# Kernel tuning notes

Hardware: AMD Instinct MI355X
Metric: run time of the kernel (lower is better)

Reference implementation:

```python
import jax, jax.numpy as jnp
import numpy as np

TOP_K = 2

def setup_inputs() -> dict:
    key = jax.random.key(0)
    k1, k2, k3 = jax.random.split(key, 3)
    B, S, H, E = 4, 4096, 4096, 64
    return {
        "hidden_states": jax.random.normal(k1, (B, S, H), dtype=jnp.float32),
        "weight": jax.random.normal(k2, (E, H), dtype=jnp.float32),
        "bias": jax.random.normal(k3, (E,), dtype=jnp.float32),
    }

def reference(hidden_states, weight, bias):
    B, S, H = hidden_states.shape
    E = weight.shape[0]
    x = hidden_states.reshape(-1, H)                      # [N, H]
    router_logits = jnp.einsum('nh,eh->ne', x, weight) + bias  # [N, E]
    routing_weights, selected_experts = jax.lax.top_k(router_logits, TOP_K)
    routing_weights = jax.nn.softmax(routing_weights.astype(jnp.float32), axis=-1).astype(hidden_states.dtype)
    N = x.shape[0]
    rows = jnp.arange(N)[:, None]
    final = jnp.zeros((N, E), dtype=router_logits.dtype).at[rows, selected_experts].set(routing_weights)
    return final.reshape(B, S, E), selected_experts
```

## Files before the change

### kernel.cpp

```cpp
#include <hip/hip_runtime.h>
#include <math.h>


constexpr int E_EXPERTS = 64;
constexpr int H_DIM = 4096;
constexpr int BLOCK = 512;
constexpr int ROWS_B = 64;
constexpr int NSTEP = 64;
constexpr int KHALF = 2048;
constexpr int SROW = 40;
constexpr int PSTR = E_EXPERTS * SROW;
constexpr int QSTR = 3 * PSTR;
constexpr int BSTR = 2 * QSTR;
constexpr int W_ELEMS = E_EXPERTS * H_DIM;

typedef __attribute__((ext_vector_type(8))) short short8;
typedef __attribute__((ext_vector_type(4))) float f32x4;

__device__ __forceinline__ float4 ld4(const float* p) {
  return *reinterpret_cast<const float4*>(p);
}
__device__ __forceinline__ short8 lds8(const unsigned short* p) {
  return *reinterpret_cast<const short8*>(p);
}

__device__ __forceinline__ unsigned short bf_rne(float x) {
  unsigned u = __builtin_bit_cast(unsigned, x);
  return (unsigned short)((u + 0x7fffu + ((u >> 16) & 1u)) >> 16);
}
__device__ __forceinline__ float bf2f(unsigned short b) {
  return __builtin_bit_cast(float, ((unsigned)b) << 16);
}
__device__ __forceinline__ void split3(float x, unsigned short& h,
                                       unsigned short& m, unsigned short& l) {
  unsigned short hb = (unsigned short)(__builtin_bit_cast(unsigned, x) >> 16);
  float r1 = x - bf2f(hb);
  unsigned short mb = (unsigned short)(__builtin_bit_cast(unsigned, r1) >> 16);
  float r2 = r1 - bf2f(mb);
  h = hb;
  m = mb;
  l = bf_rne(r2);
}
__device__ __forceinline__ void split3_8(float4 a, float4 b, short8& h,
                                         short8& m, short8& l) {
  unsigned short hh, mm, ll;
  split3(a.x, hh, mm, ll); h[0] = (short)hh; m[0] = (short)mm; l[0] = (short)ll;
  split3(a.y, hh, mm, ll); h[1] = (short)hh; m[1] = (short)mm; l[1] = (short)ll;
  split3(a.z, hh, mm, ll); h[2] = (short)hh; m[2] = (short)mm; l[2] = (short)ll;
  split3(a.w, hh, mm, ll); h[3] = (short)hh; m[3] = (short)mm; l[3] = (short)ll;
  split3(b.x, hh, mm, ll); h[4] = (short)hh; m[4] = (short)mm; l[4] = (short)ll;
  split3(b.y, hh, mm, ll); h[5] = (short)hh; m[5] = (short)mm; l[5] = (short)ll;
  split3(b.z, hh, mm, ll); h[6] = (short)hh; m[6] = (short)mm; l[6] = (short)ll;
  split3(b.w, hh, mm, ll); h[7] = (short)hh; m[7] = (short)mm; l[7] = (short)ll;
}

__global__ __launch_bounds__(256) void split_w_kernel(
    const float* __restrict__ w, unsigned short* __restrict__ wh,
    unsigned short* __restrict__ wm, unsigned short* __restrict__ wl) {
  const int i = (blockIdx.x * 256 + threadIdx.x) * 4;
  float4 v = ld4(w + i);
  ushort4 h4, m4, l4;
  split3(v.x, h4.x, m4.x, l4.x);
  split3(v.y, h4.y, m4.y, l4.y);
  split3(v.z, h4.z, m4.z, l4.z);
  split3(v.w, h4.w, m4.w, l4.w);
  *reinterpret_cast<ushort4*>(wh + i) = h4;
  *reinterpret_cast<ushort4*>(wm + i) = m4;
  *reinterpret_cast<ushort4*>(wl + i) = l4;
}

__global__ __launch_bounds__(BLOCK, 2) void topk_router_mfma(
    const float* __restrict__ x, const unsigned short* __restrict__ wh,
    const unsigned short* __restrict__ wm,
    const unsigned short* __restrict__ wl, const float* __restrict__ bias,
    float* __restrict__ out_final, float* __restrict__ out_idx) {
  __shared__ short smem[2 * BSTR];

  const int tid = threadIdx.x;
  const int lane = tid & 63;
  const int wid = tid >> 6;
  const int rg = wid & 3;
  const int kq = wid >> 2;
  const int rowBase = blockIdx.x * ROWS_B;
  const int lr = lane & 15;
  const int kg = lane >> 4;

  const int sw = tid & 255;
  const int se = sw >> 2;
  const int sk8 = tid & 3;
  const int skq = tid >> 8;
  const size_t gbase = (size_t)se * H_DIM + skq * KHALF + sk8 * 8;
  const int lbase = skq * QSTR + se * SROW + sk8 * 8;

  const float* __restrict__ xp =
      x + (size_t)(rowBase + rg * 16 + lr) * H_DIM + kq * KHALF + kg * 8;

  short8 s0, s1, s2;
  float4 xA0, xA1, xB0, xB1;

  f32x4 acc0 = {0.f, 0.f, 0.f, 0.f}, acc1 = acc0, acc2 = acc0, acc3 = acc0;

#define SLOAD(s)                        \
  do {                                  \
    const size_t go = gbase + (s) * 32; \
    s0 = lds8(wh + go);                 \
    s1 = lds8(wm + go);                 \
    s2 = lds8(wl + go);                 \
  } while (0)

#define SWRITE(buf)                                                         \
  do {                                                                      \
    *reinterpret_cast<short8*>(&smem[(buf)*BSTR + lbase + 0 * PSTR]) = s0;  \
    *reinterpret_cast<short8*>(&smem[(buf)*BSTR + lbase + 1 * PSTR]) = s1;  \
    *reinterpret_cast<short8*>(&smem[(buf)*BSTR + lbase + 2 * PSTR]) = s2;  \
  } while (0)

#define XLOAD(d0, d1, s)                  \
  do {                                    \
    d0 = ld4(xp + (size_t)(s) * 32);      \
    d1 = ld4(xp + (size_t)(s) * 32 + 4);  \
  } while (0)

  SLOAD(0);
  SWRITE(0);
  SLOAD(1);
  XLOAD(xA0, xA1, 0);
  XLOAD(xB0, xB1, 1);
  __syncthreads();

  const int fbase = kq * QSTR + lr * SROW + kg * 8;

#define FRAGS(buf, g, p)                      \
  (*reinterpret_cast<const short8*>(          \
      &smem[(buf)*BSTR + fbase + (g)*16 * SROW + (p)*PSTR]))

#define MM(d, a, b) d = __builtin_amdgcn_mfma_f32_16x16x32_bf16(a, b, d, 0, 0, 0)
#define PROD6(d, Ah, Am, Al, Bh, Bm, Bl)                      \
  MM(d, Ah, Bh); MM(d, Ah, Bm); MM(d, Am, Bh); MM(d, Am, Bm); \
  MM(d, Ah, Bl); MM(d, Al, Bh)

#define PHASE(s, buf, XF0, XF1)                                     \
  do {                                                              \
    if ((s) + 1 < NSTEP) SWRITE(1 - (buf));  \
    if ((s) + 2 < NSTEP) SLOAD((s) + 2);     \
    short8 b0h = FRAGS(buf, 0, 0), b0m = FRAGS(buf, 0, 1),          \
           b0l = FRAGS(buf, 0, 2);                                  \
    short8 b1h = FRAGS(buf, 1, 0), b1m = FRAGS(buf, 1, 1),          \
           b1l = FRAGS(buf, 1, 2);                                  \
    short8 b2h = FRAGS(buf, 2, 0), b2m = FRAGS(buf, 2, 1),          \
           b2l = FRAGS(buf, 2, 2);                                  \
    short8 b3h = FRAGS(buf, 3, 0), b3m = FRAGS(buf, 3, 1),          \
           b3l = FRAGS(buf, 3, 2);                                  \
    short8 ah, am, al;                                              \
    split3_8(XF0, XF1, ah, am, al);                                 \
    if ((s) + 2 < NSTEP) XLOAD(XF0, XF1, (s) + 2);                  \
    PROD6(acc0, ah, am, al, b0h, b0m, b0l);                         \
    PROD6(acc1, ah, am, al, b1h, b1m, b1l);                         \
    PROD6(acc2, ah, am, al, b2h, b2m, b2l);                         \
    PROD6(acc3, ah, am, al, b3h, b3m, b3l);                         \
    __syncthreads();                                                \
  } while (0)

  for (int s = 0; s < NSTEP; s += 2) {
    PHASE(s, 0, xA0, xA1);
    PHASE(s + 1, 1, xB0, xB1);
  }

  float* part = reinterpret_cast<float*>(smem);
  const int pr = kg * 4;
#define PSTORE(A, g)                                                       \
  part[((size_t)kq * 64 + rg * 16 + pr + 0) * 68 + (g)*16 + lr] = A[0];    \
  part[((size_t)kq * 64 + rg * 16 + pr + 1) * 68 + (g)*16 + lr] = A[1];    \
  part[((size_t)kq * 64 + rg * 16 + pr + 2) * 68 + (g)*16 + lr] = A[2];    \
  part[((size_t)kq * 64 + rg * 16 + pr + 3) * 68 + (g)*16 + lr] = A[3];
  PSTORE(acc0, 0)
  PSTORE(acc1, 1)
  PSTORE(acc2, 2)
  PSTORE(acc3, 3)
  __syncthreads();

  const int r = tid >> 3;
  const int eb = (tid & 7) * 8;
  const int n = rowBase + r;

  float v8[8];
#pragma unroll
  for (int j = 0; j < 8; ++j) {
    int e = eb + j;
    v8[j] = (part[(size_t)r * 68 + e] + part[(size_t)(64 + r) * 68 + e]) +
            bias[e];
  }

  float av = -INFINITY, bv = -INFINITY;
  int ai = E_EXPERTS, bi = E_EXPERTS;
#pragma unroll
  for (int j = 0; j < 8; ++j) {
    int e = eb + j;
    float v = v8[j];
    bool beats_a = (v > av) || (v == av && e < ai);
    bool beats_b = (v > bv) || (v == bv && e < bi);
    if (beats_a) {
      bv = av; bi = ai; av = v; ai = e;
    } else if (beats_b) {
      bv = v; bi = e;
    }
  }
#pragma unroll
  for (int d = 1; d < 8; d <<= 1) {
    float av2 = __shfl_xor(av, d);
    float bv2 = __shfl_xor(bv, d);
    int ai2 = __shfl_xor(ai, d);
    int bi2 = __shfl_xor(bi, d);
    bool afirst = (av > av2) || (av == av2 && ai < ai2);
    float na, nb;
    int nai, nbi;
    if (afirst) {
      na = av; nai = ai;
      bool t = (bv > av2) || (bv == av2 && bi < ai2);
      nb = t ? bv : av2;
      nbi = t ? bi : ai2;
    } else {
      na = av2; nai = ai2;
      bool t = (av > bv2) || (av == bv2 && ai < bi2);
      nb = t ? av : bv2;
      nbi = t ? ai : bi2;
    }
    av = na; ai = nai; bv = nb; bi = nbi;
  }

  float e1 = expf(bv - av);
  float denom = 1.0f + e1;
  float p0 = 1.0f / denom;
  float p1 = e1 / denom;

#pragma unroll
  for (int i = 0; i < 2; ++i) {
    float4 o4;
    float* po = &o4.x;
#pragma unroll
    for (int j = 0; j < 4; ++j) {
      int e = eb + i * 4 + j;
      po[j] = (e == ai) ? p0 : (e == bi) ? p1 : 0.0f;
    }
    *reinterpret_cast<float4*>(&out_final[(size_t)n * E_EXPERTS + eb + i * 4]) =
        o4;
  }
  if ((tid & 7) == 0) {
    out_idx[(size_t)n * 2 + 0] = (float)ai;
    out_idx[(size_t)n * 2 + 1] = (float)bi;
  }
}

extern "C" void kernel_launch(void* const* d_in, const int* in_sizes, int n_in,
                              void* d_out, int out_size, void* d_ws,
                              size_t ws_size, hipStream_t stream) {
  const float* x = (const float*)d_in[0];
  const float* w = (const float*)d_in[1];
  const float* bias = (const float*)d_in[2];
  const int N = in_sizes[0] / H_DIM;
  float* out_final = (float*)d_out;
  float* out_idx = out_final + (size_t)N * E_EXPERTS;

  unsigned short* wh = (unsigned short*)d_ws;
  unsigned short* wm = wh + W_ELEMS;
  unsigned short* wl = wm + W_ELEMS;

  split_w_kernel<<<W_ELEMS / (256 * 4), 256, 0, stream>>>(w, wh, wm, wl);
  topk_router_mfma<<<N / ROWS_B, BLOCK, 0, stream>>>(x, wh, wm, wl, bias,
                                                     out_final, out_idx);
}
```

Measured before the change: 102.6 us.

## Drop LDS weight staging; read split weights directly from global per wave

Blocks shrink to 16 rows and 256 threads, with each of 4 waves covering a 1024-wide K slice. Each wave loads the bf16 hi/mid/lo weight fragments straight from global memory (L2-resident) instead of staging them through double-buffered LDS with barriers. This removes the LDS writes and the per-step __syncthreads, and raises the block count from 256 to 1024. The cost is much less weight reuse per block: each block rereads the full split weight from cache, so L2 traffic grows by about 4x. The partial sums are reduced across 4 K-slices and the top-k shuffle reduction now spans 16 lanes.

```diff
diff --git a/kernel.cpp b/kernel.cpp
--- a/kernel.cpp
+++ b/kernel.cpp
@@ -4,14 +4,10 @@
 
 constexpr int E_EXPERTS = 64;
 constexpr int H_DIM = 4096;
-constexpr int BLOCK = 512;
-constexpr int ROWS_B = 64;
-constexpr int NSTEP = 64;
-constexpr int KHALF = 2048;
-constexpr int SROW = 40;
-constexpr int PSTR = E_EXPERTS * SROW;
-constexpr int QSTR = 3 * PSTR;
-constexpr int BSTR = 2 * QSTR;
+constexpr int BLOCK = 256;
+constexpr int ROWS_B = 16;
+constexpr int KSLICE = 1024;
+constexpr int NCH = 32;
 constexpr int W_ELEMS = E_EXPERTS * H_DIM;
 
 typedef __attribute__((ext_vector_type(8))) short short8;
@@ -69,134 +65,154 @@
   *reinterpret_cast<ushort4*>(wl + i) = l4;
 }
 
-__global__ __launch_bounds__(BLOCK, 2) void topk_router_mfma(
+__global__ __launch_bounds__(BLOCK, 4) void topk_router_mfma(
     const float* __restrict__ x, const unsigned short* __restrict__ wh,
     const unsigned short* __restrict__ wm,
     const unsigned short* __restrict__ wl, const float* __restrict__ bias,
     float* __restrict__ out_final, float* __restrict__ out_idx) {
-  __shared__ short smem[2 * BSTR];
+  __shared__ float part[4 * ROWS_B * 68];
 
   const int tid = threadIdx.x;
   const int lane = tid & 63;
-  const int wid = tid >> 6;
-  const int rg = wid & 3;
-  const int kq = wid >> 2;
+  const int kq = tid >> 6;
   const int rowBase = blockIdx.x * ROWS_B;
   const int lr = lane & 15;
   const int kg = lane >> 4;
 
-  const int sw = tid & 255;
-  const int se = sw >> 2;
-  const int sk8 = tid & 3;
-  const int skq = tid >> 8;
-  const size_t gbase = (size_t)se * H_DIM + skq * KHALF + sk8 * 8;
-  const int lbase = skq * QSTR + se * SROW + sk8 * 8;
-
-  const float* __restrict__ xp =
-      x + (size_t)(rowBase + rg * 16 + lr) * H_DIM + kq * KHALF + kg * 8;
-
-  short8 s0, s1, s2;
+  const size_t wo = (size_t)lr * H_DIM + kq * KSLICE + kg * 8;
+  const unsigned short* __restrict__ whp = wh + wo;
+  const unsigned short* __restrict__ wmp = wm + wo;
+  const unsigned short* __restrict__ wlp = wl + wo;
+
+  const float* __restrict__ xr =
+      x + (size_t)(rowBase + lr) * H_DIM + kq * KSLICE + kg * 8;
+
   float4 xA0, xA1, xB0, xB1;
+#define XLOADA(t)                         \
+  do {                                    \
+    xA0 = ld4(xr + (size_t)(t) * 32);     \
+    xA1 = ld4(xr + (size_t)(t) * 32 + 4); \
+  } while (0)
+#define XLOADB(t)                         \
+  do {                                    \
+    xB0 = ld4(xr + (size_t)(t) * 32);     \
+    xB1 = ld4(xr + (size_t)(t) * 32 + 4); \
+  } while (0)
 
   f32x4 acc0 = {0.f, 0.f, 0.f, 0.f}, acc1 = acc0, acc2 = acc0, acc3 = acc0;
-
-#define SLOAD(s)                        \
-  do {                                  \
-    const size_t go = gbase + (s) * 32; \
-    s0 = lds8(wh + go);                 \
-    s1 = lds8(wm + go);                 \
-    s2 = lds8(wl + go);                 \
-  } while (0)
-
-#define SWRITE(buf)                                                         \
-  do {                                                                      \
-    *reinterpret_cast<short8*>(&smem[(buf)*BSTR + lbase + 0 * PSTR]) = s0;  \
-    *reinterpret_cast<short8*>(&smem[(buf)*BSTR + lbase + 1 * PSTR]) = s1;  \
-    *reinterpret_cast<short8*>(&smem[(buf)*BSTR + lbase + 2 * PSTR]) = s2;  \
-  } while (0)
-
-#define XLOAD(d0, d1, s)                  \
-  do {                                    \
-    d0 = ld4(xp + (size_t)(s) * 32);      \
-    d1 = ld4(xp + (size_t)(s) * 32 + 4);  \
-  } while (0)
-
-  SLOAD(0);
-  SWRITE(0);
-  SLOAD(1);
-  XLOAD(xA0, xA1, 0);
-  XLOAD(xB0, xB1, 1);
-  __syncthreads();
-
-  const int fbase = kq * QSTR + lr * SROW + kg * 8;
-
-#define FRAGS(buf, g, p)                      \
-  (*reinterpret_cast<const short8*>(          \
-      &smem[(buf)*BSTR + fbase + (g)*16 * SROW + (p)*PSTR]))
 
 #define MM(d, a, b) d = __builtin_amdgcn_mfma_f32_16x16x32_bf16(a, b, d, 0, 0, 0)
 #define PROD6(d, Ah, Am, Al, Bh, Bm, Bl)                      \
   MM(d, Ah, Bh); MM(d, Ah, Bm); MM(d, Am, Bh); MM(d, Am, Bm); \
   MM(d, Ah, Bl); MM(d, Al, Bh)
 
-#define PHASE(s, buf, XF0, XF1)                                     \
-  do {                                                              \
-    if ((s) + 1 < NSTEP) SWRITE(1 - (buf));  \
-    if ((s) + 2 < NSTEP) SLOAD((s) + 2);     \
-    short8 b0h = FRAGS(buf, 0, 0), b0m = FRAGS(buf, 0, 1),          \
-           b0l = FRAGS(buf, 0, 2);                                  \
-    short8 b1h = FRAGS(buf, 1, 0), b1m = FRAGS(buf, 1, 1),          \
-           b1l = FRAGS(buf, 1, 2);                                  \
-    short8 b2h = FRAGS(buf, 2, 0), b2m = FRAGS(buf, 2, 1),          \
-           b2l = FRAGS(buf, 2, 2);                                  \
-    short8 b3h = FRAGS(buf, 3, 0), b3m = FRAGS(buf, 3, 1),          \
-           b3l = FRAGS(buf, 3, 2);                                  \
-    short8 ah, am, al;                                              \
-    split3_8(XF0, XF1, ah, am, al);                                 \
-    if ((s) + 2 < NSTEP) XLOAD(XF0, XF1, (s) + 2);                  \
-    PROD6(acc0, ah, am, al, b0h, b0m, b0l);                         \
-    PROD6(acc1, ah, am, al, b1h, b1m, b1l);                         \
-    PROD6(acc2, ah, am, al, b2h, b2m, b2l);                         \
-    PROD6(acc3, ah, am, al, b3h, b3m, b3l);                         \
-    __syncthreads();                                                \
+#define CHUNK(c, X0, X1)                                           \
+  do {                                                             \
+    const size_t o_ = (size_t)(c) * 32;                            \
+    short8 b0h = lds8(whp + o_);                                   \
+    short8 b1h = lds8(whp + o_ + (size_t)16 * H_DIM);              \
+    short8 b2h = lds8(whp + o_ + (size_t)32 * H_DIM);              \
+    short8 b3h = lds8(whp + o_ + (size_t)48 * H_DIM);              \
+    short8 b0m = lds8(wmp + o_);                                   \
+    short8 b1m = lds8(wmp + o_ + (size_t)16 * H_DIM);              \
+    short8 b2m = lds8(wmp + o_ + (size_t)32 * H_DIM);              \
+    short8 b3m = lds8(wmp + o_ + (size_t)48 * H_DIM);              \
+    short8 b0l = lds8(wlp + o_);                                   \
+    short8 b1l = lds8(wlp + o_ + (size_t)16 * H_DIM);              \
+    short8 b2l = lds8(wlp + o_ + (size_t)32 * H_DIM);              \
+    short8 b3l = lds8(wlp + o_ + (size_t)48 * H_DIM);              \
+    short8 ah, am, al;                                             \
+    split3_8(X0, X1, ah, am, al);                                  \
+    PROD6(acc0, ah, am, al, b0h, b0m, b0l);                        \
+    PROD6(acc1, ah, am, al, b1h, b1m, b1l);                        \
+    PROD6(acc2, ah, am, al, b2h, b2m, b2l);                        \
+    PROD6(acc3, ah, am, al, b3h, b3m, b3l);                        \
   } while (0)
 
-  for (int s = 0; s < NSTEP; s += 2) {
-    PHASE(s, 0, xA0, xA1);
-    PHASE(s + 1, 1, xB0, xB1);
-  }
-
-  float* part = reinterpret_cast<float*>(smem);
+  XLOADA(0);
+  XLOADB(1);
+
+  for (int c = 0; c < NCH; c += 2) {
+    {
+      const size_t o_ = (size_t)c * 32;
+      short8 b0h = lds8(whp + o_);
+      short8 b1h = lds8(whp + o_ + (size_t)16 * H_DIM);
+      short8 b2h = lds8(whp + o_ + (size_t)32 * H_DIM);
+      short8 b3h = lds8(whp + o_ + (size_t)48 * H_DIM);
+      short8 b0m = lds8(wmp + o_);
+      short8 b1m = lds8(wmp + o_ + (size_t)16 * H_DIM);
+      short8 b2m = lds8(wmp + o_ + (size_t)32 * H_DIM);
+      short8 b3m = lds8(wmp + o_ + (size_t)48 * H_DIM);
+      short8 b0l = lds8(wlp + o_);
+      short8 b1l = lds8(wlp + o_ + (size_t)16 * H_DIM);
+      short8 b2l = lds8(wlp + o_ + (size_t)32 * H_DIM);
+      short8 b3l = lds8(wlp + o_ + (size_t)48 * H_DIM);
+      short8 ah, am, al;
+      split3_8(xA0, xA1, ah, am, al);
+      if (c + 2 < NCH) XLOADA(c + 2);
+      PROD6(acc0, ah, am, al, b0h, b0m, b0l);
+      PROD6(acc1, ah, am, al, b1h, b1m, b1l);
+      PROD6(acc2, ah, am, al, b2h, b2m, b2l);
+      PROD6(acc3, ah, am, al, b3h, b3m, b3l);
+    }
+    {
+      const size_t o_ = (size_t)(c + 1) * 32;
+      short8 b0h = lds8(whp + o_);
+      short8 b1h = lds8(whp + o_ + (size_t)16 * H_DIM);
+      short8 b2h = lds8(whp + o_ + (size_t)32 * H_DIM);
+      short8 b3h = lds8(whp + o_ + (size_t)48 * H_DIM);
+      short8 b0m = lds8(wmp + o_);
+      short8 b1m = lds8(wmp + o_ + (size_t)16 * H_DIM);
+      short8 b2m = lds8(wmp + o_ + (size_t)32 * H_DIM);
+      short8 b3m = lds8(wmp + o_ + (size_t)48 * H_DIM);
+      short8 b0l = lds8(wlp + o_);
+      short8 b1l = lds8(wlp + o_ + (size_t)16 * H_DIM);
+      short8 b2l = lds8(wlp + o_ + (size_t)32 * H_DIM);
+      short8 b3l = lds8(wlp + o_ + (size_t)48 * H_DIM);
+      short8 ah, am, al;
+      split3_8(xB0, xB1, ah, am, al);
+      if (c + 3 < NCH) XLOADB(c + 3);
+      PROD6(acc0, ah, am, al, b0h, b0m, b0l);
+      PROD6(acc1, ah, am, al, b1h, b1m, b1l);
+      PROD6(acc2, ah, am, al, b2h, b2m, b2l);
+      PROD6(acc3, ah, am, al, b3h, b3m, b3l);
+    }
+  }
+
   const int pr = kg * 4;
-#define PSTORE(A, g)                                                       \
-  part[((size_t)kq * 64 + rg * 16 + pr + 0) * 68 + (g)*16 + lr] = A[0];    \
-  part[((size_t)kq * 64 + rg * 16 + pr + 1) * 68 + (g)*16 + lr] = A[1];    \
-  part[((size_t)kq * 64 + rg * 16 + pr + 2) * 68 + (g)*16 + lr] = A[2];    \
-  part[((size_t)kq * 64 + rg * 16 + pr + 3) * 68 + (g)*16 + lr] = A[3];
+#define PSTORE(A, g)                                          \
+  part[(size_t)(kq * 16 + pr + 0) * 68 + (g)*16 + lr] = A[0]; \
+  part[(size_t)(kq * 16 + pr + 1) * 68 + (g)*16 + lr] = A[1]; \
+  part[(size_t)(kq * 16 + pr + 2) * 68 + (g)*16 + lr] = A[2]; \
+  part[(size_t)(kq * 16 + pr + 3) * 68 + (g)*16 + lr] = A[3];
   PSTORE(acc0, 0)
   PSTORE(acc1, 1)
   PSTORE(acc2, 2)
   PSTORE(acc3, 3)
   __syncthreads();
 
-  const int r = tid >> 3;
-  const int eb = (tid & 7) * 8;
+  const int r = tid >> 4;
+  const int te = tid & 15;
+  const int eb = te * 4;
   const int n = rowBase + r;
 
-  float v8[8];
-#pragma unroll
-  for (int j = 0; j < 8; ++j) {
+  float v4[4];
+#pragma unroll
+  for (int j = 0; j < 4; ++j) {
     int e = eb + j;
-    v8[j] = (part[(size_t)r * 68 + e] + part[(size_t)(64 + r) * 68 + e]) +
+    v4[j] = ((part[(size_t)(0 * 16 + r) * 68 + e] +
+              part[(size_t)(1 * 16 + r) * 68 + e]) +
+             (part[(size_t)(2 * 16 + r) * 68 + e] +
+              part[(size_t)(3 * 16 + r) * 68 + e])) +
             bias[e];
   }
 
   float av = -INFINITY, bv = -INFINITY;
   int ai = E_EXPERTS, bi = E_EXPERTS;
 #pragma unroll
-  for (int j = 0; j < 8; ++j) {
+  for (int j = 0; j < 4; ++j) {
     int e = eb + j;
-    float v = v8[j];
+    float v = v4[j];
     bool beats_a = (v > av) || (v == av && e < ai);
     bool beats_b = (v > bv) || (v == bv && e < bi);
     if (beats_a) {
@@ -206,7 +222,7 @@
     }
   }
 #pragma unroll
-  for (int d = 1; d < 8; d <<= 1) {
+  for (int d = 1; d < 16; d <<= 1) {
     float av2 = __shfl_xor(av, d);
     float bv2 = __shfl_xor(bv, d);
     int ai2 = __shfl_xor(ai, d);
@@ -233,19 +249,17 @@
   float p0 = 1.0f / denom;
   float p1 = e1 / denom;
 
-#pragma unroll
-  for (int i = 0; i < 2; ++i) {
+  {
     float4 o4;
     float* po = &o4.x;
 #pragma unroll
     for (int j = 0; j < 4; ++j) {
-      int e = eb + i * 4 + j;
+      int e = eb + j;
       po[j] = (e == ai) ? p0 : (e == bi) ? p1 : 0.0f;
     }
-    *reinterpret_cast<float4*>(&out_final[(size_t)n * E_EXPERTS + eb + i * 4]) =
-        o4;
-  }
-  if ((tid & 7) == 0) {
+    *reinterpret_cast<float4*>(&out_final[(size_t)n * E_EXPERTS + eb]) = o4;
+  }
+  if (te == 0) {
     out_idx[(size_t)n * 2 + 0] = (float)ai;
     out_idx[(size_t)n * 2 + 1] = (float)bi;
   }
```

New measurement: 219.9 us. +114.4%, slower.

## Split K across all eight waves with per-wave async LDS staging of weight planes

Applied to the files above, without the earlier changes.

Each of the 8 waves now owns a 512-wide K slice and computes the full 64x64 tile with 16 accumulators, instead of 4 row groups by 2 K halves. Weight hi/mid planes are copied straight into per-wave LDS buffers with global_load_lds and explicit vmcnt waits. The low plane is read directly from global, and block-wide syncs inside the loop are dropped. Partial sums from all eight K slices are reduced in shared memory at the end. The goal is less sync overhead and more reuse of A and B fragments per wave, at the cost of higher register pressure and a bigger final reduction.

```diff
diff --git a/kernel.cpp b/kernel.cpp
--- a/kernel.cpp
+++ b/kernel.cpp
@@ -6,13 +6,11 @@
 constexpr int H_DIM = 4096;
 constexpr int BLOCK = 512;
 constexpr int ROWS_B = 64;
-constexpr int NSTEP = 64;
-constexpr int KHALF = 2048;
-constexpr int SROW = 40;
-constexpr int PSTR = E_EXPERTS * SROW;
-constexpr int QSTR = 3 * PSTR;
-constexpr int BSTR = 2 * QSTR;
+constexpr int KSLICE = 512;
+constexpr int NCH = 16;
 constexpr int W_ELEMS = E_EXPERTS * H_DIM;
+constexpr int TILE_SH = 8 * 512;
+constexpr int WAVE_SH = 2 * TILE_SH;
 
 typedef __attribute__((ext_vector_type(8))) short short8;
 typedef __attribute__((ext_vector_type(4))) float f32x4;
@@ -22,6 +20,12 @@
 }
 __device__ __forceinline__ short8 lds8(const unsigned short* p) {
   return *reinterpret_cast<const short8*>(p);
+}
+__device__ __forceinline__ void gload16(const unsigned short* g,
+                                        unsigned short* l) {
+  __builtin_amdgcn_global_load_lds(
+      (const __attribute__((address_space(1))) void*)g,
+      (__attribute__((address_space(3))) void*)l, 16, 0, 0);
 }
 
 __device__ __forceinline__ unsigned short bf_rne(float x) {
@@ -70,113 +74,143 @@
 }
 
 __global__ __launch_bounds__(BLOCK, 2) void topk_router_mfma(
-    const float* __restrict__ x, const unsigned short* __restrict__ wh,
-    const unsigned short* __restrict__ wm,
-    const unsigned short* __restrict__ wl, const float* __restrict__ bias,
-    float* __restrict__ out_final, float* __restrict__ out_idx) {
-  __shared__ short smem[2 * BSTR];
+    const float* __restrict__ x, const unsigned short* __restrict__ wplanes,
+    const float* __restrict__ bias, float* __restrict__ out_final,
+    float* __restrict__ out_idx) {
+  __shared__ f32x4 smem4[8704];
+  unsigned short* sbase = reinterpret_cast<unsigned short*>(smem4);
+  float* part = reinterpret_cast<float*>(smem4);
 
   const int tid = threadIdx.x;
   const int lane = tid & 63;
-  const int wid = tid >> 6;
-  const int rg = wid & 3;
-  const int kq = wid >> 2;
+  const int kq = tid >> 6;
   const int rowBase = blockIdx.x * ROWS_B;
   const int lr = lane & 15;
   const int kg = lane >> 4;
 
-  const int sw = tid & 255;
-  const int se = sw >> 2;
-  const int sk8 = tid & 3;
-  const int skq = tid >> 8;
-  const size_t gbase = (size_t)se * H_DIM + skq * KHALF + sk8 * 8;
-  const int lbase = skq * QSTR + se * SROW + sk8 * 8;
-
-  const float* __restrict__ xp =
-      x + (size_t)(rowBase + rg * 16 + lr) * H_DIM + kq * KHALF + kg * 8;
-
-  short8 s0, s1, s2;
-  float4 xA0, xA1, xB0, xB1;
-
-  f32x4 acc0 = {0.f, 0.f, 0.f, 0.f}, acc1 = acc0, acc2 = acc0, acc3 = acc0;
-
-#define SLOAD(s)                        \
-  do {                                  \
-    const size_t go = gbase + (s) * 32; \
-    s0 = lds8(wh + go);                 \
-    s1 = lds8(wm + go);                 \
-    s2 = lds8(wl + go);                 \
+  unsigned short* lb = sbase + kq * WAVE_SH;
+
+  const unsigned short* __restrict__ wb =
+      wplanes + (size_t)lr * H_DIM + kq * KSLICE + kg * 8;
+  const unsigned short* __restrict__ wlb = wb + (size_t)2 * W_ELEMS;
+
+#define STAGE(t, buf)                                                       \
+  do {                                                                      \
+    const size_t o_ = (size_t)(t) * 32;                                     \
+    unsigned short* d_ = lb + (buf)*TILE_SH;                                \
+    gload16(wb + o_, d_ + 0 * 512);                                         \
+    gload16(wb + o_ + (size_t)W_ELEMS, d_ + 1 * 512);                       \
+    gload16(wb + o_ + (size_t)16 * H_DIM, d_ + 2 * 512);                    \
+    gload16(wb + o_ + (size_t)16 * H_DIM + (size_t)W_ELEMS, d_ + 3 * 512);  \
+    gload16(wb + o_ + (size_t)32 * H_DIM, d_ + 4 * 512);                    \
+    gload16(wb + o_ + (size_t)32 * H_DIM + (size_t)W_ELEMS, d_ + 5 * 512);  \
+    gload16(wb + o_ + (size_t)48 * H_DIM, d_ + 6 * 512);                    \
+    gload16(wb + o_ + (size_t)48 * H_DIM + (size_t)W_ELEMS, d_ + 7 * 512);  \
   } while (0)
 
-#define SWRITE(buf)                                                         \
-  do {                                                                      \
-    *reinterpret_cast<short8*>(&smem[(buf)*BSTR + lbase + 0 * PSTR]) = s0;  \
-    *reinterpret_cast<short8*>(&smem[(buf)*BSTR + lbase + 1 * PSTR]) = s1;  \
-    *reinterpret_cast<short8*>(&smem[(buf)*BSTR + lbase + 2 * PSTR]) = s2;  \
+  const float* __restrict__ xr0 =
+      x + (size_t)(rowBase + lr) * H_DIM + kq * KSLICE + kg * 8;
+  const float* __restrict__ xr1 = xr0 + (size_t)16 * H_DIM;
+  const float* __restrict__ xr2 = xr0 + (size_t)32 * H_DIM;
+  const float* __restrict__ xr3 = xr0 + (size_t)48 * H_DIM;
+
+  float4 xA00, xA01, xA10, xA11, xA20, xA21, xA30, xA31;
+  float4 xB00, xB01, xB10, xB11, xB20, xB21, xB30, xB31;
+#define XLOADA(t)                                                         \
+  do {                                                                    \
+    xA00 = ld4(xr0 + (size_t)(t) * 32); xA01 = ld4(xr0 + (size_t)(t) * 32 + 4); \
+    xA10 = ld4(xr1 + (size_t)(t) * 32); xA11 = ld4(xr1 + (size_t)(t) * 32 + 4); \
+    xA20 = ld4(xr2 + (size_t)(t) * 32); xA21 = ld4(xr2 + (size_t)(t) * 32 + 4); \
+    xA30 = ld4(xr3 + (size_t)(t) * 32); xA31 = ld4(xr3 + (size_t)(t) * 32 + 4); \
   } while (0)
-
-#define XLOAD(d0, d1, s)                  \
-  do {                                    \
-    d0 = ld4(xp + (size_t)(s) * 32);      \
-    d1 = ld4(xp + (size_t)(s) * 32 + 4);  \
+#define XLOADB(t)                                                         \
+  do {                                                                    \
+    xB00 = ld4(xr0 + (size_t)(t) * 32); xB01 = ld4(xr0 + (size_t)(t) * 32 + 4); \
+    xB10 = ld4(xr1 + (size_t)(t) * 32); xB11 = ld4(xr1 + (size_t)(t) * 32 + 4); \
+    xB20 = ld4(xr2 + (size_t)(t) * 32); xB21 = ld4(xr2 + (size_t)(t) * 32 + 4); \
+    xB30 = ld4(xr3 + (size_t)(t) * 32); xB31 = ld4(xr3 + (size_t)(t) * 32 + 4); \
   } while (0)
 
-  SLOAD(0);
-  SWRITE(0);
-  SLOAD(1);
-  XLOAD(xA0, xA1, 0);
-  XLOAD(xB0, xB1, 1);
-  __syncthreads();
-
-  const int fbase = kq * QSTR + lr * SROW + kg * 8;
-
-#define FRAGS(buf, g, p)                      \
-  (*reinterpret_cast<const short8*>(          \
-      &smem[(buf)*BSTR + fbase + (g)*16 * SROW + (p)*PSTR]))
+  f32x4 c00 = {0.f, 0.f, 0.f, 0.f}, c01 = c00, c02 = c00, c03 = c00,
+        c10 = c00, c11 = c00, c12 = c00, c13 = c00, c20 = c00, c21 = c00,
+        c22 = c00, c23 = c00, c30 = c00, c31 = c00, c32 = c00, c33 = c00;
 
 #define MM(d, a, b) d = __builtin_amdgcn_mfma_f32_16x16x32_bf16(a, b, d, 0, 0, 0)
 #define PROD6(d, Ah, Am, Al, Bh, Bm, Bl)                      \
   MM(d, Ah, Bh); MM(d, Ah, Bm); MM(d, Am, Bh); MM(d, Am, Bm); \
   MM(d, Ah, Bl); MM(d, Al, Bh)
 
-#define PHASE(s, buf, XF0, XF1)                                     \
-  do {                                                              \
-    if ((s) + 1 < NSTEP) SWRITE(1 - (buf));  \
-    if ((s) + 2 < NSTEP) SLOAD((s) + 2);     \
-    short8 b0h = FRAGS(buf, 0, 0), b0m = FRAGS(buf, 0, 1),          \
-           b0l = FRAGS(buf, 0, 2);                                  \
-    short8 b1h = FRAGS(buf, 1, 0), b1m = FRAGS(buf, 1, 1),          \
-           b1l = FRAGS(buf, 1, 2);                                  \
-    short8 b2h = FRAGS(buf, 2, 0), b2m = FRAGS(buf, 2, 1),          \
-           b2l = FRAGS(buf, 2, 2);                                  \
-    short8 b3h = FRAGS(buf, 3, 0), b3m = FRAGS(buf, 3, 1),          \
-           b3l = FRAGS(buf, 3, 2);                                  \
-    short8 ah, am, al;                                              \
-    split3_8(XF0, XF1, ah, am, al);                                 \
-    if ((s) + 2 < NSTEP) XLOAD(XF0, XF1, (s) + 2);                  \
-    PROD6(acc0, ah, am, al, b0h, b0m, b0l);                         \
-    PROD6(acc1, ah, am, al, b1h, b1m, b1l);                         \
-    PROD6(acc2, ah, am, al, b2h, b2m, b2l);                         \
-    PROD6(acc3, ah, am, al, b3h, b3m, b3l);                         \
-    __syncthreads();                                                \
+  STAGE(0, 0);
+  XLOADA(0);
+  XLOADB(1);
+
+#define BODY(c, X00, X01, X10, X11, X20, X21, X30, X31, XLOADM)              \
+  do {                                                                       \
+    if ((c) + 1 < NCH) STAGE((c) + 1, ((c) + 1) & 1);                        \
+    const size_t wo_ = (size_t)(c) * 32;                                     \
+    short8 bl0 = lds8(wlb + wo_);                                            \
+    short8 bl1 = lds8(wlb + wo_ + (size_t)16 * H_DIM);                       \
+    short8 bl2 = lds8(wlb + wo_ + (size_t)32 * H_DIM);                       \
+    short8 bl3 = lds8(wlb + wo_ + (size_t)48 * H_DIM);                       \
+    __builtin_amdgcn_sched_barrier(0);                                       \
+    if ((c) == 0) {                                                          \
+      asm volatile("s_waitcnt vmcnt(28)" ::: "memory");                      \
+    } else if ((c) <= 14) {                                                  \
+      asm volatile("s_waitcnt vmcnt(20)" ::: "memory");                      \
+    } else {                                                                 \
+      asm volatile("s_waitcnt vmcnt(0)" ::: "memory");                       \
+    }                                                                        \
+    __builtin_amdgcn_sched_barrier(0);                                       \
+    const unsigned short* tb_ = lb + ((c)&1) * TILE_SH;                      \
+    short8 b0h = lds8(tb_ + 0 * 512 + lane * 8);                             \
+    short8 b0m = lds8(tb_ + 1 * 512 + lane * 8);                             \
+    short8 b1h = lds8(tb_ + 2 * 512 + lane * 8);                             \
+    short8 b1m = lds8(tb_ + 3 * 512 + lane * 8);                             \
+    short8 b2h = lds8(tb_ + 4 * 512 + lane * 8);                             \
+    short8 b2m = lds8(tb_ + 5 * 512 + lane * 8);                             \
+    short8 b3h = lds8(tb_ + 6 * 512 + lane * 8);                             \
+    short8 b3m = lds8(tb_ + 7 * 512 + lane * 8);                             \
+    short8 a0h, a0m, a0l, a1h, a1m, a1l, a2h, a2m, a2l, a3h, a3m, a3l;       \
+    split3_8(X00, X01, a0h, a0m, a0l);                                       \
+    split3_8(X10, X11, a1h, a1m, a1l);                                       \
+    split3_8(X20, X21, a2h, a2m, a2l);                                       \
+    split3_8(X30, X31, a3h, a3m, a3l);                                       \
+    if ((c) + 2 < NCH) XLOADM((c) + 2);          \
+    PROD6(c00, a0h, a0m, a0l, b0h, b0m, bl0);                                \
+    PROD6(c01, a0h, a0m, a0l, b1h, b1m, bl1);                                \
+    PROD6(c02, a0h, a0m, a0l, b2h, b2m, bl2);                                \
+    PROD6(c03, a0h, a0m, a0l, b3h, b3m, bl3);                                \
+    PROD6(c10, a1h, a1m, a1l, b0h, b0m, bl0);                                \
+    PROD6(c11, a1h, a1m, a1l, b1h, b1m, bl1);                                \
+    PROD6(c12, a1h, a1m, a1l, b2h, b2m, bl2);                                \
+    PROD6(c13, a1h, a1m, a1l, b3h, b3m, bl3);                                \
+    PROD6(c20, a2h, a2m, a2l, b0h, b0m, bl0);                                \
+    PROD6(c21, a2h, a2m, a2l, b1h, b1m, bl1);                                \
+    PROD6(c22, a2h, a2m, a2l, b2h, b2m, bl2);                                \
+    PROD6(c23, a2h, a2m, a2l, b3h, b3m, bl3);                                \
+    PROD6(c30, a3h, a3m, a3l, b0h, b0m, bl0);                                \
+    PROD6(c31, a3h, a3m, a3l, b1h, b1m, bl1);                                \
+    PROD6(c32, a3h, a3m, a3l, b2h, b2m, bl2);                                \
+    PROD6(c33, a3h, a3m, a3l, b3h, b3m, bl3);                                \
   } while (0)
 
-  for (int s = 0; s < NSTEP; s += 2) {
-    PHASE(s, 0, xA0, xA1);
-    PHASE(s + 1, 1, xB0, xB1);
-  }
-
-  float* part = reinterpret_cast<float*>(smem);
+  for (int c = 0; c < NCH; c += 2) {
+    BODY(c, xA00, xA01, xA10, xA11, xA20, xA21, xA30, xA31, XLOADA);
+    BODY(c + 1, xB00, xB01, xB10, xB11, xB20, xB21, xB30, xB31, XLOADB);
+  }
+
+  __syncthreads();
+
   const int pr = kg * 4;
-#define PSTORE(A, g)                                                       \
-  part[((size_t)kq * 64 + rg * 16 + pr + 0) * 68 + (g)*16 + lr] = A[0];    \
-  part[((size_t)kq * 64 + rg * 16 + pr + 1) * 68 + (g)*16 + lr] = A[1];    \
-  part[((size_t)kq * 64 + rg * 16 + pr + 2) * 68 + (g)*16 + lr] = A[2];    \
-  part[((size_t)kq * 64 + rg * 16 + pr + 3) * 68 + (g)*16 + lr] = A[3];
-  PSTORE(acc0, 0)
-  PSTORE(acc1, 1)
-  PSTORE(acc2, 2)
-  PSTORE(acc3, 3)
+#define PST(A, af, g)                                                      \
+  part[(size_t)(kq * 64 + (af)*16 + pr + 0) * 68 + (g)*16 + lr] = A[0];    \
+  part[(size_t)(kq * 64 + (af)*16 + pr + 1) * 68 + (g)*16 + lr] = A[1];    \
+  part[(size_t)(kq * 64 + (af)*16 + pr + 2) * 68 + (g)*16 + lr] = A[2];    \
+  part[(size_t)(kq * 64 + (af)*16 + pr + 3) * 68 + (g)*16 + lr] = A[3];
+  PST(c00, 0, 0) PST(c01, 0, 1) PST(c02, 0, 2) PST(c03, 0, 3)
+  PST(c10, 1, 0) PST(c11, 1, 1) PST(c12, 1, 2) PST(c13, 1, 3)
+  PST(c20, 2, 0) PST(c21, 2, 1) PST(c22, 2, 2) PST(c23, 2, 3)
+  PST(c30, 3, 0) PST(c31, 3, 1) PST(c32, 3, 2) PST(c33, 3, 3)
   __syncthreads();
 
   const int r = tid >> 3;
@@ -187,8 +221,15 @@
 #pragma unroll
   for (int j = 0; j < 8; ++j) {
     int e = eb + j;
-    v8[j] = (part[(size_t)r * 68 + e] + part[(size_t)(64 + r) * 68 + e]) +
-            bias[e];
+    float s01 = part[(size_t)(0 * 64 + r) * 68 + e] +
+                part[(size_t)(1 * 64 + r) * 68 + e];
+    float s23 = part[(size_t)(2 * 64 + r) * 68 + e] +
+                part[(size_t)(3 * 64 + r) * 68 + e];
+    float s45 = part[(size_t)(4 * 64 + r) * 68 + e] +
+                part[(size_t)(5 * 64 + r) * 68 + e];
+    float s67 = part[(size_t)(6 * 64 + r) * 68 + e] +
+                part[(size_t)(7 * 64 + r) * 68 + e];
+    v8[j] = ((s01 + s23) + (s45 + s67)) + bias[e];
   }
 
   float av = -INFINITY, bv = -INFINITY;
@@ -266,6 +307,6 @@
   unsigned short* wl = wm + W_ELEMS;
 
   split_w_kernel<<<W_ELEMS / (256 * 4), 256, 0, stream>>>(w, wh, wm, wl);
-  topk_router_mfma<<<N / ROWS_B, BLOCK, 0, stream>>>(x, wh, wm, wl, bias,
-                                                     out_final, out_idx);
-}
+  topk_router_mfma<<<N / ROWS_B, BLOCK, 0, stream>>>(x, wh, bias, out_final,
+                                                     out_idx);
+}
```

Result: faster. 93.53 us (-8.8%).
